# Optimization experiments

Hardware: AMD Instinct MI355X
Metric: run time of the kernel (lower is better)

Reference implementation:

```python
import jax, jax.numpy as jnp
import numpy as np
import math

V, T, D, H, L, B = 50257, 1024, 768, 12, 6, 2
FF = 4 * D
HD = D // H

def layernorm(x, g, b, eps=1e-5):
    mu = jnp.mean(x, axis=-1, keepdims=True)
    var = jnp.var(x, axis=-1, keepdims=True)
    return (x - mu) * jax.lax.rsqrt(var + eps) * g + b

def new_gelu(x):
    # Faithful to the (buggy) NewGelu: tanh arg = sqrt(2/pi) * 0.044715 * x**4
    c = math.sqrt(2.0 / math.pi)
    return 0.5 * x * (1.0 + jnp.tanh(c * (x * 0.044715 * jnp.power(x, 3))))

def setup_inputs() -> dict:
    key = jax.random.key(0)
    ks = jax.random.split(key, 18)
    n = lambda k, shape, s=0.02: (jax.random.normal(k, shape, dtype=jnp.float32) * s)
    return {
        "ids": jax.random.randint(ks[0], (B, T), 0, V),
        "wte": n(ks[1], (V, D)),
        "wpe": n(ks[2], (T, D)),
        "W_qkv": n(ks[3], (L, D, 3 * D)),
        "b_qkv": jnp.zeros((L, 3 * D), jnp.float32),
        "W_o": n(ks[4], (L, D, D)),
        "b_o": jnp.zeros((L, D), jnp.float32),
        "ln1_g": jnp.ones((L, D), jnp.float32),
        "ln1_b": jnp.zeros((L, D), jnp.float32),
        "W1": n(ks[5], (L, D, FF)),
        "b1": jnp.zeros((L, FF), jnp.float32),
        "W2": n(ks[6], (L, FF, D)),
        "b2": jnp.zeros((L, D), jnp.float32),
        "lnf_g": jnp.ones((D,), jnp.float32),
        "lnf_b": jnp.zeros((D,), jnp.float32),
        "W_head": n(ks[7], (D, V)),
        "b_head": jnp.zeros((V,), jnp.float32),
    }

def reference(ids, wte, wpe, W_qkv, b_qkv, W_o, b_o, ln1_g, ln1_b,
              W1, b1, W2, b2, lnf_g, lnf_b, W_head, b_head):
    t = ids.shape[1]
    x = wte[ids] + wpe[:t][None]  # [B,T,D]
    scale = 1.0 / math.sqrt(HD)
    for l in range(L):
        qkv = x @ W_qkv[l] + b_qkv[l]                 # [B,T,3D]
        q, k, v = jnp.split(qkv, 3, axis=-1)
        q = q.reshape(-1, t, H, HD).transpose(0, 2, 1, 3)  # [B,H,T,hd]
        k = k.reshape(-1, t, H, HD).transpose(0, 2, 1, 3)
        v = v.reshape(-1, t, H, HD).transpose(0, 2, 1, 3)
        # NOTE: mask buffer is all-ones in the source, so NO causal masking.
        att = jax.nn.softmax(jnp.einsum('bhqd,bhkd->bhqk', q, k) * scale, axis=-1)
        y = jnp.einsum('bhqk,bhkd->bhqd', att, v)
        y = y.transpose(0, 2, 1, 3).reshape(-1, t, D)
        y = y @ W_o[l] + b_o[l]
        x = layernorm(y, ln1_g[l], ln1_b[l]) + x      # ln1 AFTER attn, per source
        h = new_gelu(x @ W1[l] + b1[l]) @ W2[l] + b2[l]  # ln2 unused, per source
        x = h + x
    x = layernorm(x, lnf_g, lnf_b)
    logits = x @ W_head + b_head
    return logits
```

## Files before the change

kernel.cpp:

```cpp
#include <hip/hip_runtime.h>
#include <hip/hip_bf16.h>
#include <math.h>
#include <stdint.h>

#define NL 6
#define NB 2
#define ST 1024
#define ND 768
#define NH 12
#define HD 64
#define NFF 3072
#define NV 50257
#define ND3 2304
#define NM (NB * ST)

typedef short bf16x4 __attribute__((ext_vector_type(4)));
typedef short bf16x8 __attribute__((ext_vector_type(8)));
typedef float f32x4  __attribute__((ext_vector_type(4)));

typedef __attribute__((address_space(3))) void as3_void;
typedef __attribute__((address_space(1))) void as1_void;

__device__ __forceinline__ void async_copy16(const void* g, void* lds) {
  __builtin_amdgcn_global_load_lds((const as1_void*)(uintptr_t)g,
                                   (as3_void*)(uint32_t)(uintptr_t)lds,
                                   16, 0, 0);
}

__device__ __forceinline__ unsigned short f2bf(float f) {
  union { float f; uint32_t u; } v; v.f = f;
  return (unsigned short)((v.u + 0x7fffu + ((v.u >> 16) & 1u)) >> 16);
}

__device__ __forceinline__ bf16x8 frag16(const unsigned short* p) {
  return *(const bf16x8*)p;
}

template <int N>
__device__ __forceinline__ void wait_vm_barrier() {
  if constexpr (N == 8)      asm volatile("s_waitcnt vmcnt(8)\n\ts_barrier" ::: "memory");
  else if constexpr (N == 6) asm volatile("s_waitcnt vmcnt(6)\n\ts_barrier" ::: "memory");
  else                       asm volatile("s_waitcnt vmcnt(0)\n\ts_barrier" ::: "memory");
}
__device__ __forceinline__ void lgkm_barrier() {
  asm volatile("s_waitcnt lgkmcnt(0)\n\ts_barrier" ::: "memory");
}

#define MFMA(a, b, c) __builtin_amdgcn_mfma_f32_16x16x32_bf16((a), (b), (c), 0, 0, 0)

__device__ __forceinline__ float gelu_buggy(float x) {
  const float c = 0.7978845608028654f;
  float x2 = x * x;
  return 0.5f * x * (1.0f + tanhf(c * 0.044715f * x2 * x2));
}

enum { EP_QKV = 0, EP_PROJ, EP_FF1, EP_FF2, EP_HEAD };

template <int EPI, int TM, int TN, int WN, int NW>
__global__ __launch_bounds__(NW * 64)
void gemm_bt(const unsigned short* __restrict__ A,
             const unsigned short* __restrict__ BT,
             const float* __restrict__ bias,
             float* __restrict__ Cf,
             unsigned short* __restrict__ Cb,
             const float* __restrict__ resid,
             int M, int N, int K)
{
  constexpr int WM = NW / WN;
  constexpr int FM = TM / WM / 16;
  constexpr int FN = TN / WN / 16;
  constexpr int CA = TM / 8 / NW;
  constexpr int CB = TN / 8 / NW;
  constexpr int LPT = CA + CB;
  __shared__ __align__(16) unsigned short As[2][TM * 64];
  __shared__ __align__(16) unsigned short Bs[2][TN * 64];
  const int tid = threadIdx.x;
  const int w = tid >> 6, l = tid & 63;
  const int g = l >> 4, r = l & 15;
  const int wm = (w / WN) * (FM * 16);
  const int wn = (w % WN) * (FN * 16);

  const int nbx = gridDim.x;
  const int nwg = nbx * gridDim.y;
  int bid = blockIdx.y * nbx + blockIdx.x;
  if ((nwg & 7) == 0) bid = (bid & 7) * (nwg >> 3) + (bid >> 3);
  const int m0 = (bid % nbx) * TM, n0 = (bid / nbx) * TN;

  const int sr = l >> 3;
  const int se = ((l & 7) ^ sr) * 8;
  long aoff[CA];
  long boff[CB];
#pragma unroll
  for (int c = 0; c < CA; ++c) {
    const int arow = (w * CA + c) * 8 + sr;
    aoff[c] = (long)(m0 + arow) * K + se;
  }
#pragma unroll
  for (int c = 0; c < CB; ++c) {
    int brow = n0 + (w * CB + c) * 8 + sr;
    if (brow > N - 1) brow = N - 1;
    boff[c] = (long)brow * K + se;
  }

  f32x4 acc[FM][FN] = {};

  auto stage = [&](int t, int buf) {
    const long k0 = (long)t * 64;
#pragma unroll
    for (int c = 0; c < CA; ++c)
      async_copy16(A + aoff[c] + k0, &As[buf][(w * CA + c) * 512]);
#pragma unroll
    for (int c = 0; c < CB; ++c)
      async_copy16(BT + boff[c] + k0, &Bs[buf][(w * CB + c) * 512]);
  };

  auto compute = [&](int buf) {
#pragma unroll
    for (int kk = 0; kk < 2; ++kk) {
      bf16x8 af[FM], bf[FN];
#pragma unroll
      for (int mi = 0; mi < FM; ++mi)
        af[mi] = frag16(&As[buf][(wm + mi * 16 + r) * 64 + (((kk * 4 + g) ^ (r & 7)) * 8)]);
#pragma unroll
      for (int ni = 0; ni < FN; ++ni)
        bf[ni] = frag16(&Bs[buf][(wn + ni * 16 + r) * 64 + (((kk * 4 + g) ^ (r & 7)) * 8)]);
      __builtin_amdgcn_s_setprio(1);
#pragma unroll
      for (int mi = 0; mi < FM; ++mi)
#pragma unroll
        for (int ni = 0; ni < FN; ++ni)
          acc[mi][ni] = MFMA(af[mi], bf[ni], acc[mi][ni]);
      __builtin_amdgcn_s_setprio(0);
    }
  };

  const int nt = K >> 6;
  stage(0, 0);
  for (int t = 0; t < nt - 1; ++t) {
    stage(t + 1, (t + 1) & 1);
    wait_vm_barrier<LPT>();
    compute(t & 1);
    lgkm_barrier();
  }
  wait_vm_barrier<0>();
  compute((nt - 1) & 1);

#pragma unroll
  for (int mi = 0; mi < FM; ++mi) {
#pragma unroll
    for (int ni = 0; ni < FN; ++ni) {
      const int col = n0 + wn + ni * 16 + r;
      if (EPI == EP_HEAD && col >= N) continue;
      const float bb = bias[col];
#pragma unroll
      for (int q = 0; q < 4; ++q) {
        const int row = m0 + wm + mi * 16 + g * 4 + q;
        float v = acc[mi][ni][q] + bb;
        if constexpr (EPI == EP_QKV) {
          Cb[(long)row * N + col] = f2bf(v);
        } else if constexpr (EPI == EP_PROJ) {
          Cf[(long)row * N + col] = v;
        } else if constexpr (EPI == EP_FF1) {
          Cb[(long)row * N + col] = f2bf(gelu_buggy(v));
        } else if constexpr (EPI == EP_FF2) {
          float o = v + resid[(long)row * N + col];
          Cf[(long)row * N + col] = o;
          Cb[(long)row * N + col] = f2bf(o);
        } else {
          Cf[(long)row * N + col] = v;
        }
      }
    }
  }
}

__global__ __launch_bounds__(256)
void attn_kernel(const unsigned short* __restrict__ qkv,
                 unsigned short* __restrict__ y)
{
  constexpr int LS = 72;
  __shared__ __align__(16) unsigned short Qs[64 * LS];
  __shared__ __align__(16) unsigned short Ks[64 * LS];
  __shared__ __align__(16) unsigned short Vt[64 * LS];
  __shared__ __align__(16) unsigned short Ps[64 * LS];
  const int tid = threadIdx.x;
  const int w = tid >> 6, l = tid & 63;
  const int g = l >> 4, r = l & 15;
  const int q0 = blockIdx.x * 64;
  const int b = blockIdx.y / NH, h = blockIdx.y % NH;
  const long rb = (long)b * ST;
  const int srow = tid >> 3, sc8 = (tid & 7) * 8;

#pragma unroll
  for (int p = 0; p < 2; ++p) {
    const int row = p * 32 + srow;
    bf16x8 v = *(const bf16x8*)&qkv[(rb + q0 + row) * ND3 + h * HD + sc8];
    *(bf16x8*)&Qs[row * LS + sc8] = v;
  }
  __syncthreads();
  bf16x8 aq[2];
#pragma unroll
  for (int kk = 0; kk < 2; ++kk)
    aq[kk] = *(const bf16x8*)&Qs[(w * 16 + r) * LS + kk * 32 + g * 8];

  float m_run[4] = {-1e30f, -1e30f, -1e30f, -1e30f};
  float l_run[4] = {0.f, 0.f, 0.f, 0.f};
  f32x4 acc_o[4] = {};

  for (int kt = 0; kt < ST / 64; ++kt) {
#pragma unroll
    for (int p = 0; p < 2; ++p) {
      const int row = p * 32 + srow;
      const long base = (rb + kt * 64 + row) * ND3 + h * HD + sc8;
      bf16x8 kv = *(const bf16x8*)&qkv[base + ND];
      *(bf16x8*)&Ks[row * LS + sc8] = kv;
      bf16x8 vv = *(const bf16x8*)&qkv[base + 2 * ND];
#pragma unroll
      for (int j = 0; j < 8; ++j) Vt[(sc8 + j) * LS + row] = (unsigned short)vv[j];
    }
    __syncthreads();

    f32x4 s_acc[4] = {};
#pragma unroll
    for (int kk = 0; kk < 2; ++kk) {
#pragma unroll
      for (int ni = 0; ni < 4; ++ni) {
        bf16x8 bk = *(const bf16x8*)&Ks[(ni * 16 + r) * LS + kk * 32 + g * 8];
        s_acc[ni] = MFMA(aq[kk], bk, s_acc[ni]);
      }
    }

    float mloc[4];
#pragma unroll
    for (int q = 0; q < 4; ++q) {
      float mx = fmaxf(fmaxf(s_acc[0][q], s_acc[1][q]), fmaxf(s_acc[2][q], s_acc[3][q]));
      mloc[q] = mx * 0.125f;
    }
#pragma unroll
    for (int mask = 1; mask < 16; mask <<= 1)
#pragma unroll
      for (int q = 0; q < 4; ++q)
        mloc[q] = fmaxf(mloc[q], __shfl_xor(mloc[q], mask, 64));

    float alpha[4], psum[4] = {0.f, 0.f, 0.f, 0.f};
#pragma unroll
    for (int q = 0; q < 4; ++q) {
      const float mn = fmaxf(m_run[q], mloc[q]);
      alpha[q] = __expf(m_run[q] - mn);
      m_run[q] = mn;
    }
#pragma unroll
    for (int ni = 0; ni < 4; ++ni)
#pragma unroll
      for (int q = 0; q < 4; ++q) {
        const float p = __expf(s_acc[ni][q] * 0.125f - m_run[q]);
        psum[q] += p;
        Ps[(w * 16 + g * 4 + q) * LS + ni * 16 + r] = f2bf(p);
      }
#pragma unroll
    for (int mask = 1; mask < 16; mask <<= 1)
#pragma unroll
      for (int q = 0; q < 4; ++q) psum[q] += __shfl_xor(psum[q], mask, 64);
#pragma unroll
    for (int q = 0; q < 4; ++q) l_run[q] = l_run[q] * alpha[q] + psum[q];
#pragma unroll
    for (int ni = 0; ni < 4; ++ni)
#pragma unroll
      for (int q = 0; q < 4; ++q) acc_o[ni][q] *= alpha[q];

    asm volatile("s_waitcnt lgkmcnt(0)" ::: "memory");
    __builtin_amdgcn_sched_barrier(0);

#pragma unroll
    for (int kk = 0; kk < 2; ++kk) {
      bf16x8 ap = *(const bf16x8*)&Ps[(w * 16 + r) * LS + kk * 32 + g * 8];
#pragma unroll
      for (int ni = 0; ni < 4; ++ni) {
        bf16x8 bv = *(const bf16x8*)&Vt[(ni * 16 + r) * LS + kk * 32 + g * 8];
        acc_o[ni] = MFMA(ap, bv, acc_o[ni]);
      }
    }
    __syncthreads();
  }

#pragma unroll
  for (int ni = 0; ni < 4; ++ni)
#pragma unroll
    for (int q = 0; q < 4; ++q) {
      const int row = q0 + w * 16 + g * 4 + q;
      const int col = h * HD + ni * 16 + r;
      y[(rb + row) * ND + col] = f2bf(acc_o[ni][q] / l_run[q]);
    }
}

template <bool RESID>
__global__ __launch_bounds__(256)
void ln_kernel(const float* __restrict__ in, const float* __restrict__ resid,
               const float* __restrict__ gamma, const float* __restrict__ beta,
               float* __restrict__ out_f, unsigned short* __restrict__ out_b)
{
  __shared__ float wred[8];
  const int row = blockIdx.x, tid = threadIdx.x;
  float v[3];
#pragma unroll
  for (int j = 0; j < 3; ++j) v[j] = in[(long)row * ND + tid + j * 256];
  float s = v[0] + v[1] + v[2];
#pragma unroll
  for (int m = 1; m < 64; m <<= 1) s += __shfl_xor(s, m, 64);
  if ((tid & 63) == 0) wred[tid >> 6] = s;
  __syncthreads();
  const float mean = (wred[0] + wred[1] + wred[2] + wred[3]) * (1.0f / ND);
  float d[3];
#pragma unroll
  for (int j = 0; j < 3; ++j) d[j] = v[j] - mean;
  float s2 = d[0] * d[0] + d[1] * d[1] + d[2] * d[2];
#pragma unroll
  for (int m = 1; m < 64; m <<= 1) s2 += __shfl_xor(s2, m, 64);
  if ((tid & 63) == 0) wred[4 + (tid >> 6)] = s2;
  __syncthreads();
  const float var = (wred[4] + wred[5] + wred[6] + wred[7]) * (1.0f / ND);
  const float rstd = rsqrtf(var + 1e-5f);
#pragma unroll
  for (int j = 0; j < 3; ++j) {
    const int c = tid + j * 256;
    float o = d[j] * rstd * gamma[c] + beta[c];
    if (RESID) o += resid[(long)row * ND + c];
    if (out_f) out_f[(long)row * ND + c] = o;
    if (out_b) out_b[(long)row * ND + c] = f2bf(o);
  }
}

__global__ __launch_bounds__(256)
void embed_kernel(const int* __restrict__ ids, const float* __restrict__ wte,
                  const float* __restrict__ wpe, float* __restrict__ x,
                  unsigned short* __restrict__ xb)
{
  const int t = blockIdx.x, tid = threadIdx.x;
  const int tok = ids[t];
  const int pos = t & (ST - 1);
#pragma unroll
  for (int j = 0; j < 3; ++j) {
    const int c = tid + j * 256;
    const float v = wte[(long)tok * ND + c] + wpe[(long)pos * ND + c];
    x[(long)t * ND + c] = v;
    xb[(long)t * ND + c] = f2bf(v);
  }
}

__global__ __launch_bounds__(256)
void transpose_bf16(const float* __restrict__ in, unsigned short* __restrict__ out,
                    int R, int C)
{
  __shared__ float tile[64][33];
  const long z = (long)blockIdx.z * R * C;
  const int c0 = blockIdx.x * 32, r0 = blockIdx.y * 64;
  const int tx = threadIdx.x & 31, ty = threadIdx.x >> 5;
#pragma unroll
  for (int j = 0; j < 8; ++j) {
    const int rr = r0 + j * 8 + ty, cc = c0 + tx;
    if (cc < C) tile[j * 8 + ty][tx] = in[z + (long)rr * C + cc];
  }
  __syncthreads();
  const int rx = threadIdx.x & 63, cy = threadIdx.x >> 6;
#pragma unroll
  for (int j = 0; j < 8; ++j) {
    const int cc = c0 + j * 4 + cy;
    if (cc < C) out[z + (long)cc * R + r0 + rx] = f2bf(tile[rx][j * 4 + cy]);
  }
}

extern "C" void kernel_launch(void* const* d_in, const int* in_sizes, int n_in,
                              void* d_out, int out_size, void* d_ws, size_t ws_size,
                              hipStream_t stream)
{
  const int*   ids    = (const int*)d_in[0];
  const float* wte    = (const float*)d_in[1];
  const float* wpe    = (const float*)d_in[2];
  const float* W_qkv  = (const float*)d_in[3];
  const float* b_qkv  = (const float*)d_in[4];
  const float* W_o    = (const float*)d_in[5];
  const float* b_o    = (const float*)d_in[6];
  const float* ln1_g  = (const float*)d_in[7];
  const float* ln1_b  = (const float*)d_in[8];
  const float* W1     = (const float*)d_in[9];
  const float* b1     = (const float*)d_in[10];
  const float* W2     = (const float*)d_in[11];
  const float* b2     = (const float*)d_in[12];
  const float* lnf_g  = (const float*)d_in[13];
  const float* lnf_b  = (const float*)d_in[14];
  const float* W_head = (const float*)d_in[15];
  const float* b_head = (const float*)d_in[16];
  float* out = (float*)d_out;
  (void)in_sizes; (void)n_in; (void)out_size; (void)ws_size;

  char* ws = (char*)d_ws;
  size_t off = 0;
  auto alloc = [&](size_t bytes) -> void* {
    void* p = (void*)(ws + off);
    off = (off + bytes + 255) & ~(size_t)255;
    return p;
  };
  unsigned short* wqkvT = (unsigned short*)alloc((size_t)NL * ND3 * ND * 2);
  unsigned short* woT   = (unsigned short*)alloc((size_t)NL * ND * ND * 2);
  unsigned short* w1T   = (unsigned short*)alloc((size_t)NL * NFF * ND * 2);
  unsigned short* w2T   = (unsigned short*)alloc((size_t)NL * ND * NFF * 2);
  unsigned short* whT   = (unsigned short*)alloc((size_t)NV * ND * 2);
  float*          xf    = (float*)alloc((size_t)NM * ND * 4);
  unsigned short* xb    = (unsigned short*)alloc((size_t)NM * ND * 2);
  unsigned short* qkvb  = (unsigned short*)alloc((size_t)NM * ND3 * 2);
  unsigned short* yb    = (unsigned short*)alloc((size_t)NM * ND * 2);
  float*          aof   = (float*)alloc((size_t)NM * ND * 4);
  unsigned short* h1b   = (unsigned short*)alloc((size_t)NM * NFF * 2);
  unsigned short* xlnb  = (unsigned short*)alloc((size_t)NM * ND * 2);

  dim3 tb(256);
  dim3 tb128(128);
  transpose_bf16<<<dim3(ND3 / 32, ND / 64, NL), tb, 0, stream>>>(W_qkv, wqkvT, ND, ND3);
  transpose_bf16<<<dim3(ND / 32, ND / 64, NL), tb, 0, stream>>>(W_o, woT, ND, ND);
  transpose_bf16<<<dim3(NFF / 32, ND / 64, NL), tb, 0, stream>>>(W1, w1T, ND, NFF);
  transpose_bf16<<<dim3(ND / 32, NFF / 64, NL), tb, 0, stream>>>(W2, w2T, NFF, ND);
  transpose_bf16<<<dim3((NV + 31) / 32, ND / 64, 1), tb, 0, stream>>>(W_head, whT, ND, NV);

  embed_kernel<<<dim3(NM), tb, 0, stream>>>(ids, wte, wpe, xf, xb);

  for (int l = 0; l < NL; ++l) {
    gemm_bt<EP_QKV, 128, 64, 2, 4><<<dim3(NM / 128, ND3 / 64), tb, 0, stream>>>(
        xb, wqkvT + (size_t)l * ND3 * ND, b_qkv + (size_t)l * ND3,
        nullptr, qkvb, nullptr, NM, ND3, ND);
    attn_kernel<<<dim3(ST / 64, NB * NH), tb, 0, stream>>>(qkvb, yb);
    gemm_bt<EP_PROJ, 64, 64, 2, 2><<<dim3(NM / 64, ND / 64), tb128, 0, stream>>>(
        yb, woT + (size_t)l * ND * ND, b_o + (size_t)l * ND,
        aof, nullptr, nullptr, NM, ND, ND);
    ln_kernel<true><<<dim3(NM), tb, 0, stream>>>(
        aof, xf, ln1_g + (size_t)l * ND, ln1_b + (size_t)l * ND, xf, xb);
    gemm_bt<EP_FF1, 128, 64, 2, 4><<<dim3(NM / 128, NFF / 64), tb, 0, stream>>>(
        xb, w1T + (size_t)l * NFF * ND, b1 + (size_t)l * NFF,
        nullptr, h1b, nullptr, NM, NFF, ND);
    gemm_bt<EP_FF2, 64, 64, 2, 2><<<dim3(NM / 64, ND / 64), tb128, 0, stream>>>(
        h1b, w2T + (size_t)l * ND * NFF, b2 + (size_t)l * ND,
        xf, xb, xf, NM, ND, NFF);
  }
  ln_kernel<false><<<dim3(NM), tb, 0, stream>>>(xf, nullptr, lnf_g, lnf_b, nullptr, xlnb);
  gemm_bt<EP_HEAD, 128, 128, 2, 4><<<dim3(NM / 128, (NV + 127) / 128), tb, 0, stream>>>(
      xlnb, whT, b_head, out, nullptr, nullptr, NM, NV, ND);
}
```

Measured before the change: 1.218 ms.

## Write V transposed from QKV epilogue and enlarge head GEMM tiles

The QKV GEMM epilogue now writes the V part straight into a per-head transposed buffer [B,H,HD,T]. The attention kernel can then load V^T with vector loads instead of doing scalar LDS transpose stores. The GEMM also gains a BK template parameter, and the vocab head GEMM moves to 256x256 tiles with 8 warps and BK=32 to get more reuse per block. The cost is scattered short4 stores in the epilogue, plus a larger LDS and register footprint and fewer blocks for the head GEMM.

```diff
diff --git a/kernel.cpp b/kernel.cpp
--- a/kernel.cpp
+++ b/kernel.cpp
@@ -40,6 +40,7 @@
 __device__ __forceinline__ void wait_vm_barrier() {
   if constexpr (N == 8)      asm volatile("s_waitcnt vmcnt(8)\n\ts_barrier" ::: "memory");
   else if constexpr (N == 6) asm volatile("s_waitcnt vmcnt(6)\n\ts_barrier" ::: "memory");
+  else if constexpr (N == 4) asm volatile("s_waitcnt vmcnt(4)\n\ts_barrier" ::: "memory");
   else                       asm volatile("s_waitcnt vmcnt(0)\n\ts_barrier" ::: "memory");
 }
 __device__ __forceinline__ void lgkm_barrier() {
@@ -56,7 +57,7 @@
 
 enum { EP_QKV = 0, EP_PROJ, EP_FF1, EP_FF2, EP_HEAD };
 
-template <int EPI, int TM, int TN, int WN, int NW>
+template <int EPI, int TM, int TN, int WN, int NW, int BK>
 __global__ __launch_bounds__(NW * 64)
 void gemm_bt(const unsigned short* __restrict__ A,
              const unsigned short* __restrict__ BT,
@@ -64,16 +65,20 @@
              float* __restrict__ Cf,
              unsigned short* __restrict__ Cb,
              const float* __restrict__ resid,
+             unsigned short* __restrict__ vT,
              int M, int N, int K)
 {
   constexpr int WM = NW / WN;
   constexpr int FM = TM / WM / 16;
   constexpr int FN = TN / WN / 16;
-  constexpr int CA = TM / 8 / NW;
-  constexpr int CB = TN / 8 / NW;
+  constexpr int SL = BK / 8;
+  constexpr int RPC = 1024 / (BK * 2);
+  constexpr int CA = TM / RPC / NW;
+  constexpr int CB = TN / RPC / NW;
   constexpr int LPT = CA + CB;
-  __shared__ __align__(16) unsigned short As[2][TM * 64];
-  __shared__ __align__(16) unsigned short Bs[2][TN * 64];
+  constexpr int KK = BK / 32;
+  __shared__ __align__(16) unsigned short As[2][TM * BK];
+  __shared__ __align__(16) unsigned short Bs[2][TN * BK];
   const int tid = threadIdx.x;
   const int w = tid >> 6, l = tid & 63;
   const int g = l >> 4, r = l & 15;
@@ -86,18 +91,18 @@
   if ((nwg & 7) == 0) bid = (bid & 7) * (nwg >> 3) + (bid >> 3);
   const int m0 = (bid % nbx) * TM, n0 = (bid / nbx) * TN;
 
-  const int sr = l >> 3;
-  const int se = ((l & 7) ^ sr) * 8;
+  const int sr = l / (BK / 8);
+  const int se = ((l & (SL - 1)) ^ (sr & (SL - 1))) * 8;
   long aoff[CA];
   long boff[CB];
 #pragma unroll
   for (int c = 0; c < CA; ++c) {
-    const int arow = (w * CA + c) * 8 + sr;
+    const int arow = (w * CA + c) * RPC + sr;
     aoff[c] = (long)(m0 + arow) * K + se;
   }
 #pragma unroll
   for (int c = 0; c < CB; ++c) {
-    int brow = n0 + (w * CB + c) * 8 + sr;
+    int brow = n0 + (w * CB + c) * RPC + sr;
     if (brow > N - 1) brow = N - 1;
     boff[c] = (long)brow * K + se;
   }
@@ -105,7 +110,7 @@
   f32x4 acc[FM][FN] = {};
 
   auto stage = [&](int t, int buf) {
-    const long k0 = (long)t * 64;
+    const long k0 = (long)t * BK;
 #pragma unroll
     for (int c = 0; c < CA; ++c)
       async_copy16(A + aoff[c] + k0, &As[buf][(w * CA + c) * 512]);
@@ -116,14 +121,14 @@
 
   auto compute = [&](int buf) {
 #pragma unroll
-    for (int kk = 0; kk < 2; ++kk) {
+    for (int kk = 0; kk < KK; ++kk) {
       bf16x8 af[FM], bf[FN];
 #pragma unroll
       for (int mi = 0; mi < FM; ++mi)
-        af[mi] = frag16(&As[buf][(wm + mi * 16 + r) * 64 + (((kk * 4 + g) ^ (r & 7)) * 8)]);
+        af[mi] = frag16(&As[buf][(wm + mi * 16 + r) * BK + (((kk * 4 + g) ^ (r & (SL - 1))) * 8)]);
 #pragma unroll
       for (int ni = 0; ni < FN; ++ni)
-        bf[ni] = frag16(&Bs[buf][(wn + ni * 16 + r) * 64 + (((kk * 4 + g) ^ (r & 7)) * 8)]);
+        bf[ni] = frag16(&Bs[buf][(wn + ni * 16 + r) * BK + (((kk * 4 + g) ^ (r & (SL - 1))) * 8)]);
       __builtin_amdgcn_s_setprio(1);
 #pragma unroll
       for (int mi = 0; mi < FM; ++mi)
@@ -134,7 +139,7 @@
     }
   };
 
-  const int nt = K >> 6;
+  const int nt = K / BK;
   stage(0, 0);
   for (int t = 0; t < nt - 1; ++t) {
     stage(t + 1, (t + 1) & 1);
@@ -152,6 +157,17 @@
       const int col = n0 + wn + ni * 16 + r;
       if (EPI == EP_HEAD && col >= N) continue;
       const float bb = bias[col];
+      if (EPI == EP_QKV && col >= 2 * ND) {
+        const int hv = (col - 2 * ND) >> 6, d = (col - 2 * ND) & 63;
+        short4 vv;
+#pragma unroll
+        for (int q = 0; q < 4; ++q)
+          vv[q] = (short)f2bf(acc[mi][ni][q] + bb);
+        const int row = m0 + wm + mi * 16 + g * 4;
+        const int bb_ = row >> 10, t4 = row & 1023;
+        *(short4*)&vT[(((long)bb_ * NH + hv) * HD + d) * ST + t4] = vv;
+        continue;
+      }
 #pragma unroll
       for (int q = 0; q < 4; ++q) {
         const int row = m0 + wm + mi * 16 + g * 4 + q;
@@ -176,6 +192,7 @@
 
 __global__ __launch_bounds__(256)
 void attn_kernel(const unsigned short* __restrict__ qkv,
+                 const unsigned short* __restrict__ vT,
                  unsigned short* __restrict__ y)
 {
   constexpr int LS = 72;
@@ -189,6 +206,7 @@
   const int q0 = blockIdx.x * 64;
   const int b = blockIdx.y / NH, h = blockIdx.y % NH;
   const long rb = (long)b * ST;
+  const long vbase = ((long)b * NH + h) * HD * ST;
   const int srow = tid >> 3, sc8 = (tid & 7) * 8;
 
 #pragma unroll
@@ -211,12 +229,10 @@
 #pragma unroll
     for (int p = 0; p < 2; ++p) {
       const int row = p * 32 + srow;
-      const long base = (rb + kt * 64 + row) * ND3 + h * HD + sc8;
-      bf16x8 kv = *(const bf16x8*)&qkv[base + ND];
-      *(bf16x8*)&Ks[row * LS + sc8] = kv;
-      bf16x8 vv = *(const bf16x8*)&qkv[base + 2 * ND];
-#pragma unroll
-      for (int j = 0; j < 8; ++j) Vt[(sc8 + j) * LS + row] = (unsigned short)vv[j];
+      *(bf16x8*)&Ks[row * LS + sc8] =
+          *(const bf16x8*)&qkv[(rb + kt * 64 + row) * ND3 + ND + h * HD + sc8];
+      *(bf16x8*)&Vt[row * LS + sc8] =
+          *(const bf16x8*)&vT[vbase + (long)row * ST + kt * 64 + sc8];
     }
     __syncthreads();
 
@@ -412,9 +428,11 @@
   float*          aof   = (float*)alloc((size_t)NM * ND * 4);
   unsigned short* h1b   = (unsigned short*)alloc((size_t)NM * NFF * 2);
   unsigned short* xlnb  = (unsigned short*)alloc((size_t)NM * ND * 2);
+  unsigned short* vtb   = (unsigned short*)alloc((size_t)NB * NH * HD * ST * 2);
 
   dim3 tb(256);
   dim3 tb128(128);
+  dim3 tb512(512);
   transpose_bf16<<<dim3(ND3 / 32, ND / 64, NL), tb, 0, stream>>>(W_qkv, wqkvT, ND, ND3);
   transpose_bf16<<<dim3(ND / 32, ND / 64, NL), tb, 0, stream>>>(W_o, woT, ND, ND);
   transpose_bf16<<<dim3(NFF / 32, ND / 64, NL), tb, 0, stream>>>(W1, w1T, ND, NFF);
@@ -424,23 +442,23 @@
   embed_kernel<<<dim3(NM), tb, 0, stream>>>(ids, wte, wpe, xf, xb);
 
   for (int l = 0; l < NL; ++l) {
-    gemm_bt<EP_QKV, 128, 64, 2, 4><<<dim3(NM / 128, ND3 / 64), tb, 0, stream>>>(
+    gemm_bt<EP_QKV, 128, 64, 2, 4, 64><<<dim3(NM / 128, ND3 / 64), tb, 0, stream>>>(
         xb, wqkvT + (size_t)l * ND3 * ND, b_qkv + (size_t)l * ND3,
-        nullptr, qkvb, nullptr, NM, ND3, ND);
-    attn_kernel<<<dim3(ST / 64, NB * NH), tb, 0, stream>>>(qkvb, yb);
-    gemm_bt<EP_PROJ, 64, 64, 2, 2><<<dim3(NM / 64, ND / 64), tb128, 0, stream>>>(
+        nullptr, qkvb, nullptr, vtb, NM, ND3, ND);
+    attn_kernel<<<dim3(ST / 64, NB * NH), tb, 0, stream>>>(qkvb, vtb, yb);
+    gemm_bt<EP_PROJ, 64, 64, 2, 2, 64><<<dim3(NM / 64, ND / 64), tb128, 0, stream>>>(
         yb, woT + (size_t)l * ND * ND, b_o + (size_t)l * ND,
-        aof, nullptr, nullptr, NM, ND, ND);
+        aof, nullptr, nullptr, nullptr, NM, ND, ND);
     ln_kernel<true><<<dim3(NM), tb, 0, stream>>>(
         aof, xf, ln1_g + (size_t)l * ND, ln1_b + (size_t)l * ND, xf, xb);
-    gemm_bt<EP_FF1, 128, 64, 2, 4><<<dim3(NM / 128, NFF / 64), tb, 0, stream>>>(
+    gemm_bt<EP_FF1, 128, 64, 2, 4, 64><<<dim3(NM / 128, NFF / 64), tb, 0, stream>>>(
         xb, w1T + (size_t)l * NFF * ND, b1 + (size_t)l * NFF,
-        nullptr, h1b, nullptr, NM, NFF, ND);
-    gemm_bt<EP_FF2, 64, 64, 2, 2><<<dim3(NM / 64, ND / 64), tb128, 0, stream>>>(
+        nullptr, h1b, nullptr, nullptr, NM, NFF, ND);
+    gemm_bt<EP_FF2, 64, 64, 2, 2, 64><<<dim3(NM / 64, ND / 64), tb128, 0, stream>>>(
         h1b, w2T + (size_t)l * ND * NFF, b2 + (size_t)l * ND,
-        xf, xb, xf, NM, ND, NFF);
+        xf, xb, xf, nullptr, NM, ND, NFF);
   }
   ln_kernel<false><<<dim3(NM), tb, 0, stream>>>(xf, nullptr, lnf_g, lnf_b, nullptr, xlnb);
-  gemm_bt<EP_HEAD, 128, 128, 2, 4><<<dim3(NM / 128, (NV + 127) / 128), tb, 0, stream>>>(
-      xlnb, whT, b_head, out, nullptr, nullptr, NM, NV, ND);
-}
+  gemm_bt<EP_HEAD, 256, 256, 4, 8, 32><<<dim3(NM / 256, (NV + 255) / 256), tb512, 0, stream>>>(
+      xlnb, whT, b_head, out, nullptr, nullptr, nullptr, NM, NV, ND);
+}
```

Result: faster. 1.145 ms (-6.0%).
